# Performance work log

Hardware: AMD Instinct MI355X
Metric: run time of the kernel (lower is better)

## Reference

```python
import jax, jax.numpy as jnp
import numpy as np

TOP_K = 2

def setup_inputs() -> dict:
    key = jax.random.key(0)
    ks = jax.random.split(key, 6)
    B, L, D, E = 4, 4096, 1024, 8
    s = 1.0 / np.sqrt(D)
    return {
        "x": jax.random.normal(ks[0], (B, L, D), dtype=jnp.float32),
        "Wr": jax.random.normal(ks[1], (E, D), dtype=jnp.float32) * s,
        "W1": jax.random.normal(ks[2], (E, D, D), dtype=jnp.float32) * s,
        "b1": jax.random.normal(ks[3], (E, D), dtype=jnp.float32) * 0.01,
        "W2": jax.random.normal(ks[4], (E, D, D), dtype=jnp.float32) * s,
        "b2": jax.random.normal(ks[5], (E, D), dtype=jnp.float32) * 0.01,
    }

def reference(x, Wr, W1, b1, W2, b2):
    # x: [B,L,D]; Wr: [E,D]; W1/W2: [E,D,D]; b1/b2: [E,D]
    E = Wr.shape[0]
    logits = jnp.einsum("bld,ed->ble", x, Wr)           # router, no bias
    probs = jax.nn.softmax(logits, axis=-1)
    topw, topi = jax.lax.top_k(probs, TOP_K)             # [B,L,K]
    topw = topw / jnp.sum(topw, axis=-1, keepdims=True)  # renormalize
    # combine weights per expert: [B,L,E], zero where expert not selected
    comb = jnp.sum(jax.nn.one_hot(topi, E, dtype=x.dtype) * topw[..., None], axis=-2)
    out = jnp.zeros_like(x)
    for e in range(E):  # small fixed expert count
        h = jax.nn.gelu(jnp.einsum("bld,fd->blf", x, W1[e]) + b1[e], approximate=False)
        y = jnp.einsum("blf,df->bld", h, W2[e]) + b2[e]
        out = out + comb[..., e:e + 1] * y
    return out
```

## Files before the change

### kernel.cpp

```cpp
#include <hip/hip_runtime.h>
#include <hip/hip_bf16.h>
#include <cstdint>
#include <cstddef>

#define NTOK 16384
#define DDIM 1024
#define NEXP 8
#define CPAD 32

typedef __attribute__((ext_vector_type(8))) short bf16x8;
typedef __attribute__((ext_vector_type(4))) float f32x4;

__device__ __forceinline__ unsigned short f2bf(float f) {
  union { float f; unsigned u; } c; c.f = f;
  unsigned r = (c.u + 0x7FFFu + ((c.u >> 16) & 1u)) >> 16;
  return (unsigned short)r;
}

__device__ __forceinline__ float gelu_exact(float v) {
  return 0.5f * v * (1.0f + erff(v * 0.70710678118654752440f));
}

#define GL2LDS(gp, lp) __builtin_amdgcn_global_load_lds( \
    (__attribute__((address_space(1))) void*)(gp),       \
    (__attribute__((address_space(3))) void*)(lp), 16, 0, 0)

__global__ void cast_k(const float* __restrict__ src, unsigned short* __restrict__ dst, int n4) {
  int i = blockIdx.x * blockDim.x + threadIdx.x;
  if (i >= n4) return;
  float4 a = ((const float4*)src)[i];
  union { unsigned short s[4]; uint2 v; } o;
  o.s[0] = f2bf(a.x); o.s[1] = f2bf(a.y); o.s[2] = f2bf(a.z); o.s[3] = f2bf(a.w);
  ((uint2*)dst)[i] = o.v;
}

__global__ __launch_bounds__(256)
void castx_router_k(const float* __restrict__ x, const float* __restrict__ Wr,
                    unsigned short* __restrict__ xb, int* __restrict__ tokE,
                    float2* __restrict__ tokW) {
  const int t = blockIdx.x;
  const int tid = threadIdx.x;
  const int w = tid >> 6, lane = tid & 63;

  float4 xv = ((const float4*)x)[(size_t)t * 256 + tid];
  union { unsigned short s[4]; uint2 v; } o;
  o.s[0] = f2bf(xv.x); o.s[1] = f2bf(xv.y); o.s[2] = f2bf(xv.z); o.s[3] = f2bf(xv.w);
  ((uint2*)xb)[(size_t)t * 256 + tid] = o.v;

  const float4* Wr4 = (const float4*)Wr;
  float p[NEXP];
#pragma unroll
  for (int e = 0; e < NEXP; ++e) {
    float4 wv = Wr4[e * 256 + tid];
    p[e] = xv.x * wv.x + xv.y * wv.y + xv.z * wv.z + xv.w * wv.w;
  }
#pragma unroll
  for (int e = 0; e < NEXP; ++e) {
    float v = p[e];
#pragma unroll
    for (int off = 32; off >= 1; off >>= 1) v += __shfl_xor(v, off, 64);
    p[e] = v;
  }
  __shared__ float red[4][NEXP];
  if (lane == 0) {
#pragma unroll
    for (int e = 0; e < NEXP; ++e) red[w][e] = p[e];
  }
  __syncthreads();
  if (tid == 0) {
    float s[NEXP];
#pragma unroll
    for (int e = 0; e < NEXP; ++e) s[e] = red[0][e] + red[1][e] + red[2][e] + red[3][e];
    int e1 = 0; float m1 = s[0];
#pragma unroll
    for (int e = 1; e < NEXP; ++e) if (s[e] > m1) { m1 = s[e]; e1 = e; }
    int e2 = -1; float m2 = -3.4e38f;
#pragma unroll
    for (int e = 0; e < NEXP; ++e) {
      if (e == e1) continue;
      if (s[e] > m2) { m2 = s[e]; e2 = e; }
    }
    float dd = expf(m2 - m1);
    tokE[t] = e1 | (e2 << 8);
    tokW[t] = make_float2(1.f / (1.f + dd), dd / (1.f + dd));
  }
}

__global__ __launch_bounds__(256)
void hist_k(const int* __restrict__ tokE, int* __restrict__ cnt) {
  const int t = blockIdx.x * blockDim.x + threadIdx.x;
  const int w = threadIdx.x >> 6, lane = threadIdx.x & 63;
  const int pk = tokE[t];
  const int e1 = pk & 0xFF, e2 = (pk >> 8) & 0xFF;
  __shared__ int h[4][NEXP];
#pragma unroll
  for (int e = 0; e < NEXP; ++e) {
    int c = (int)__popcll(__ballot(e1 == e)) + (int)__popcll(__ballot(e2 == e));
    if (lane == 0) h[w][e] = c;
  }
  __syncthreads();
  if (threadIdx.x < NEXP) {
    int tot = h[0][threadIdx.x] + h[1][threadIdx.x] + h[2][threadIdx.x] + h[3][threadIdx.x];
    atomicAdd(&cnt[threadIdx.x * CPAD], tot);
  }
}

__global__ void offsets_k(const int* __restrict__ cnt, int* __restrict__ off) {
  if (threadIdx.x == 0) {
    int a = 0;
    for (int e = 0; e < NEXP; ++e) { off[e] = a; a += cnt[e * CPAD]; }
  }
}

__device__ __forceinline__ int bucket_slot(int* cur, int e_sel) {
  int lane = threadIdx.x & 63;
  int slot = 0;
#pragma unroll
  for (int e = 0; e < NEXP; ++e) {
    unsigned long long m = __ballot(e_sel == e);
    if (e_sel == e) {
      unsigned long long below = m & ((1ull << lane) - 1ull);
      int leader = __ffsll((long long)m) - 1;
      int base = 0;
      if (lane == leader) base = atomicAdd(&cur[e * CPAD], (int)__popcll(m));
      base = __shfl(base, leader, 64);
      slot = base + (int)__popcll(below);
    }
  }
  return slot;
}

__global__ __launch_bounds__(256)
void place_k(const int* __restrict__ tokE, const float2* __restrict__ tokW,
             const int* __restrict__ off, int* __restrict__ cur,
             int* __restrict__ asgT, float* __restrict__ asgW) {
  int t = blockIdx.x * blockDim.x + threadIdx.x;
  if (t >= NTOK) return;
  int pk = tokE[t];
  float2 w = tokW[t];
  int e1 = pk & 0xFF, e2 = (pk >> 8) & 0xFF;
  int p1 = off[e1] + bucket_slot(cur, e1);
  asgT[p1] = t; asgW[p1] = w.x;
  int p2 = off[e2] + bucket_slot(cur, e2);
  asgT[p2] = t; asgW[p2] = w.y;
}


__global__ __launch_bounds__(512, 2)
void gemm1_k(const unsigned short* __restrict__ xb, const unsigned short* __restrict__ w1b,
             const float* __restrict__ b1, const int* __restrict__ cntp,
             const int* __restrict__ offp, const int* __restrict__ asgT,
             unsigned short* __restrict__ h) {
  const int e = blockIdx.z;
  const int cnt = cntp[e * CPAD];
  const int m0 = blockIdx.x * 256;
  if (m0 >= cnt) return;
  const int off = offp[e];
  const int n0 = blockIdx.y * 256;

  __shared__ __align__(16) unsigned short As[2][16384];
  __shared__ __align__(16) unsigned short Bs[2][16384];

  const int tid = threadIdx.x;
  const int w = tid >> 6, lane = tid & 63;
  const int r = lane & 15, kc = lane >> 4;
  const int wr = w >> 2, wc = w & 3;

  const unsigned short* srcA[2];
  const unsigned short* srcB[2];
#pragma unroll
  for (int i = 0; i < 2; ++i) {
    int g = 2 * w + i;
    int rowt = m0 + g * 16 + r;
    int rowc = (rowt < cnt) ? rowt : m0;
    int tok = asgT[off + rowc];
    srcA[i] = xb + (size_t)tok * DDIM + kc * 8;
    int coln = n0 + g * 16 + r;
    srcB[i] = w1b + (size_t)e * DDIM * DDIM + (size_t)coln * DDIM + kc * 8;
  }

  f32x4 acc[8][4];
#pragma unroll
  for (int i = 0; i < 8; ++i)
#pragma unroll
    for (int j = 0; j < 4; ++j) acc[i][j] = (f32x4){0.f, 0.f, 0.f, 0.f};

  auto stage = [&](int buf, int k0) {
#pragma unroll
    for (int i = 0; i < 2; ++i) {
      int g = 2 * w + i;
#pragma unroll
      for (int ks = 0; ks < 2; ++ks) {
        GL2LDS(srcA[i] + k0 + ks * 32, &As[buf][g * 1024 + ks * 512 + lane * 8]);
        GL2LDS(srcB[i] + k0 + ks * 32, &Bs[buf][g * 1024 + ks * 512 + lane * 8]);
      }
    }
  };

  stage(0, 0);
  for (int s = 0; s < 16; ++s) {
    int buf = s & 1;
    __syncthreads();
    if (s + 1 < 16) stage(buf ^ 1, (s + 1) * 64);
#pragma unroll
    for (int ks = 0; ks < 2; ++ks) {
      bf16x8 af[8], bv[4];
#pragma unroll
      for (int i = 0; i < 8; ++i)
        af[i] = *(const bf16x8*)&As[buf][(wr * 8 + i) * 1024 + ks * 512 + lane * 8];
#pragma unroll
      for (int j = 0; j < 4; ++j)
        bv[j] = *(const bf16x8*)&Bs[buf][(wc * 4 + j) * 1024 + ks * 512 + lane * 8];
#pragma unroll
      for (int i = 0; i < 8; ++i)
#pragma unroll
        for (int j = 0; j < 4; ++j)
          acc[i][j] = __builtin_amdgcn_mfma_f32_16x16x32_bf16(af[i], bv[j], acc[i][j], 0, 0, 0);
    }
  }

  float bcol[4];
#pragma unroll
  for (int j = 0; j < 4; ++j) bcol[j] = b1[e * DDIM + n0 + wc * 64 + j * 16 + r];
#pragma unroll
  for (int i = 0; i < 8; ++i) {
#pragma unroll
    for (int q = 0; q < 4; ++q) {
      int grow = m0 + wr * 128 + i * 16 + kc * 4 + q;
      if (grow < cnt) {
        size_t hrow = (size_t)(off + grow) * DDIM;
#pragma unroll
        for (int j = 0; j < 4; ++j) {
          int col = n0 + wc * 64 + j * 16 + r;
          h[hrow + col] = f2bf(gelu_exact(acc[i][j][q] + bcol[j]));
        }
      }
    }
  }
}

__global__ __launch_bounds__(512, 2)
void gemm2_k(const unsigned short* __restrict__ hsrc, const unsigned short* __restrict__ w2b,
             const float* __restrict__ b2, const int* __restrict__ cntp,
             const int* __restrict__ offp, const int* __restrict__ asgT,
             const float* __restrict__ asgW, float* __restrict__ out) {
  const int e = blockIdx.z;
  const int cnt = cntp[e * CPAD];
  const int m0 = blockIdx.x * 256;
  if (m0 >= cnt) return;
  const int off = offp[e];
  const int n0 = blockIdx.y * 256;

  __shared__ __align__(16) unsigned short As[2][16384];
  __shared__ __align__(16) unsigned short Bs[2][16384];

  const int tid = threadIdx.x;
  const int w = tid >> 6, lane = tid & 63;
  const int r = lane & 15, kc = lane >> 4;
  const int wr = w >> 2, wc = w & 3;

  const unsigned short* srcA[2];
  const unsigned short* srcB[2];
#pragma unroll
  for (int i = 0; i < 2; ++i) {
    int g = 2 * w + i;
    int rowt = m0 + g * 16 + r;
    int rowc = (rowt < cnt) ? rowt : m0;
    srcA[i] = hsrc + (size_t)(off + rowc) * DDIM + kc * 8;
    int coln = n0 + g * 16 + r;
    srcB[i] = w2b + (size_t)e * DDIM * DDIM + (size_t)coln * DDIM + kc * 8;
  }

  f32x4 acc[8][4];
#pragma unroll
  for (int i = 0; i < 8; ++i)
#pragma unroll
    for (int j = 0; j < 4; ++j) acc[i][j] = (f32x4){0.f, 0.f, 0.f, 0.f};

  auto stage = [&](int buf, int k0) {
#pragma unroll
    for (int i = 0; i < 2; ++i) {
      int g = 2 * w + i;
#pragma unroll
      for (int ks = 0; ks < 2; ++ks) {
        GL2LDS(srcA[i] + k0 + ks * 32, &As[buf][g * 1024 + ks * 512 + lane * 8]);
        GL2LDS(srcB[i] + k0 + ks * 32, &Bs[buf][g * 1024 + ks * 512 + lane * 8]);
      }
    }
  };

  stage(0, 0);
  for (int s = 0; s < 16; ++s) {
    int buf = s & 1;
    __syncthreads();
    if (s + 1 < 16) stage(buf ^ 1, (s + 1) * 64);
#pragma unroll
    for (int ks = 0; ks < 2; ++ks) {
      bf16x8 af[8], bv[4];
#pragma unroll
      for (int i = 0; i < 8; ++i)
        af[i] = *(const bf16x8*)&As[buf][(wr * 8 + i) * 1024 + ks * 512 + lane * 8];
#pragma unroll
      for (int j = 0; j < 4; ++j)
        bv[j] = *(const bf16x8*)&Bs[buf][(wc * 4 + j) * 1024 + ks * 512 + lane * 8];
#pragma unroll
      for (int i = 0; i < 8; ++i)
#pragma unroll
        for (int j = 0; j < 4; ++j)
          acc[i][j] = __builtin_amdgcn_mfma_f32_16x16x32_bf16(af[i], bv[j], acc[i][j], 0, 0, 0);
    }
  }

  float bcol[4];
#pragma unroll
  for (int j = 0; j < 4; ++j) bcol[j] = b2[e * DDIM + n0 + wc * 64 + j * 16 + r];
#pragma unroll
  for (int i = 0; i < 8; ++i) {
#pragma unroll
    for (int q = 0; q < 4; ++q) {
      int grow = m0 + wr * 128 + i * 16 + kc * 4 + q;
      if (grow < cnt) {
        int tok = asgT[off + grow];
        float wgt = asgW[off + grow];
        float* orow = out + (size_t)tok * DDIM;
#pragma unroll
        for (int j = 0; j < 4; ++j) {
          int col = n0 + wc * 64 + j * 16 + r;
          atomicAdd(&orow[col], wgt * (acc[i][j][q] + bcol[j]));
        }
      }
    }
  }
}

extern "C" void kernel_launch(void* const* d_in, const int* in_sizes, int n_in,
                              void* d_out, int out_size, void* d_ws, size_t ws_size,
                              hipStream_t stream) {
  (void)in_sizes; (void)n_in; (void)ws_size;
  const float* x  = (const float*)d_in[0];
  const float* Wr = (const float*)d_in[1];
  const float* W1 = (const float*)d_in[2];
  const float* b1 = (const float*)d_in[3];
  const float* W2 = (const float*)d_in[4];
  const float* b2 = (const float*)d_in[5];
  float* out = (float*)d_out;

  char* ws = (char*)d_ws;
  int*    cnt  = (int*)(ws + 0);
  int*    off  = (int*)(ws + 4096);
  int*    cur  = (int*)(ws + 8192);
  int*    tokE = (int*)(ws + 16384);
  float2* tokW = (float2*)(ws + 16384 + 65536);
  int*    asgT = (int*)(ws + 16384 + 65536 + 131072);
  float*  asgW = (float*)(ws + 16384 + 65536 + 131072 + 131072);
  unsigned short* xb  = (unsigned short*)(ws + (size_t)(1u << 20));
  unsigned short* w1b = (unsigned short*)(ws + (size_t)33 * (1u << 20));
  unsigned short* w2b = (unsigned short*)(ws + (size_t)49 * (1u << 20));
  unsigned short* h   = (unsigned short*)(ws + (size_t)65 * (1u << 20));

  hipMemsetAsync(ws, 0, 16384, stream);
  hipMemsetAsync(d_out, 0, (size_t)out_size * sizeof(float), stream);

  const int nW = NEXP * DDIM * DDIM;
  cast_k<<<(nW / 4) / 256, 256, 0, stream>>>(W1, w1b, nW / 4);
  cast_k<<<(nW / 4) / 256, 256, 0, stream>>>(W2, w2b, nW / 4);

  castx_router_k<<<NTOK, 256, 0, stream>>>(x, Wr, xb, tokE, tokW);
  hist_k<<<NTOK / 256, 256, 0, stream>>>(tokE, cnt);
  offsets_k<<<1, 64, 0, stream>>>(cnt, off);
  place_k<<<NTOK / 256, 256, 0, stream>>>(tokE, tokW, off, cur, asgT, asgW);

  dim3 ggrid(64, 4, NEXP);
  gemm1_k<<<ggrid, 512, 0, stream>>>(xb, w1b, b1, cnt, off, asgT, h);
  gemm2_k<<<ggrid, 512, 0, stream>>>(h, w2b, b2, cnt, off, asgT, asgW, out);
}
```

Before: 715.4 us.

## Restructure MoE GEMM mainloop with explicit barriers, phased LDS reads and setprio

Both expert GEMM kernels now share a macro-generated mainloop. Each K-tile waits explicitly on vmcnt and a raw s_barrier, loads B fragments for both k-substeps once, then walks A fragments in four phases of two rows. Each MFMA cluster is raised with s_setprio and separated by barriers so LDS reads and MFMA issue interleave across waves. The aim is to cut register pressure from holding all eight A fragments and to overlap global-to-LDS prefetch and LDS reads with matrix math. The cost is many extra workgroup barriers per tile, which could serialize waves.

```diff
diff --git a/kernel.cpp b/kernel.cpp
--- a/kernel.cpp
+++ b/kernel.cpp
@@ -146,191 +146,168 @@
 }
 
 
+#define GEMM_CORE(EPILOG_PRE, SRC_A_INIT)                                               \
+  const int e = blockIdx.z;                                                             \
+  const int cnt = cntp[e * CPAD];                                                       \
+  const int m0 = blockIdx.x * 256;                                                      \
+  if (m0 >= cnt) return;                                                                \
+  const int off = offp[e];                                                              \
+  const int n0 = blockIdx.y * 256;                                                      \
+  __shared__ __align__(16) unsigned short As[2][16384];                                 \
+  __shared__ __align__(16) unsigned short Bs[2][16384];                                 \
+  const int tid = threadIdx.x;                                                          \
+  const int w = tid >> 6, lane = tid & 63;                                              \
+  const int r = lane & 15, kc = lane >> 4;                                              \
+  const int wr = w >> 2, wc = w & 3;                                                    \
+  const unsigned short* srcA[2];                                                        \
+  const unsigned short* srcB[2];                                                        \
+  _Pragma("unroll")                                                                     \
+  for (int i = 0; i < 2; ++i) {                                                         \
+    int g = 2 * w + i;                                                                  \
+    int rowt = m0 + g * 16 + r;                                                         \
+    int rowc = (rowt < cnt) ? rowt : m0;                                                \
+    SRC_A_INIT;                                                                         \
+    int coln = n0 + g * 16 + r;                                                         \
+    srcB[i] = Bsrc + (size_t)e * DDIM * DDIM + (size_t)coln * DDIM + kc * 8;            \
+  }                                                                                     \
+  f32x4 acc[8][4];                                                                      \
+  _Pragma("unroll")                                                                     \
+  for (int i = 0; i < 8; ++i)                                                           \
+    _Pragma("unroll")                                                                   \
+    for (int j = 0; j < 4; ++j) acc[i][j] = (f32x4){0.f, 0.f, 0.f, 0.f};                \
+  auto stage = [&](int buf, int kt) {                                                   \
+    _Pragma("unroll")                                                                   \
+    for (int i = 0; i < 2; ++i) {                                                       \
+      int g = 2 * w + i;                                                                \
+      _Pragma("unroll")                                                                 \
+      for (int ks = 0; ks < 2; ++ks) {                                                  \
+        GL2LDS(srcA[i] + kt * 64 + ks * 32, &As[buf][(g * 2 + ks) * 512 + lane * 8]);   \
+        GL2LDS(srcB[i] + kt * 64 + ks * 32, &Bs[buf][(g * 2 + ks) * 512 + lane * 8]);   \
+      }                                                                                 \
+    }                                                                                   \
+  };                                                                                    \
+  stage(0, 0);                                                                          \
+  for (int t = 0; t < 16; ++t) {                                                        \
+    const int b = t & 1;                                                                \
+    __builtin_amdgcn_sched_barrier(0);                                                  \
+    asm volatile("s_waitcnt vmcnt(0)" ::: "memory");                                    \
+    __builtin_amdgcn_s_barrier();                                                       \
+    __builtin_amdgcn_sched_barrier(0);                                                  \
+    bf16x8 bv[4][2], af[2][2];                                                          \
+    _Pragma("unroll")                                                                   \
+    for (int j = 0; j < 4; ++j)                                                         \
+      _Pragma("unroll")                                                                 \
+      for (int ks = 0; ks < 2; ++ks)                                                    \
+        bv[j][ks] = *(const bf16x8*)&Bs[b][((wc * 4 + j) * 2 + ks) * 512 + lane * 8];   \
+    _Pragma("unroll")                                                                   \
+    for (int i = 0; i < 2; ++i)                                                         \
+      _Pragma("unroll")                                                                 \
+      for (int ks = 0; ks < 2; ++ks)                                                    \
+        af[i][ks] = *(const bf16x8*)&As[b][((wr * 8 + i) * 2 + ks) * 512 + lane * 8];   \
+    if (t + 1 < 16) stage(b ^ 1, t + 1);                                                \
+    __builtin_amdgcn_s_barrier();                                                       \
+    asm volatile("s_waitcnt lgkmcnt(0)" ::: "memory");                                  \
+    __builtin_amdgcn_sched_barrier(0);                                                  \
+    __builtin_amdgcn_s_setprio(1);                                                      \
+    _Pragma("unroll")                                                                   \
+    for (int ks = 0; ks < 2; ++ks)                                                      \
+      _Pragma("unroll")                                                                 \
+      for (int i = 0; i < 2; ++i)                                                       \
+        _Pragma("unroll")                                                               \
+        for (int j = 0; j < 4; ++j)                                                     \
+          acc[i][j] = __builtin_amdgcn_mfma_f32_16x16x32_bf16(af[i][ks], bv[j][ks],     \
+                                                              acc[i][j], 0, 0, 0);      \
+    __builtin_amdgcn_s_setprio(0);                                                      \
+    __builtin_amdgcn_s_barrier();                                                       \
+    _Pragma("unroll")                                                                   \
+    for (int p = 1; p < 4; ++p) {                                                       \
+      _Pragma("unroll")                                                                 \
+      for (int i = 0; i < 2; ++i)                                                       \
+        _Pragma("unroll")                                                               \
+        for (int ks = 0; ks < 2; ++ks)                                                  \
+          af[i][ks] = *(const bf16x8*)&As[b][((wr * 8 + 2 * p + i) * 2 + ks) * 512 +    \
+                                             lane * 8];                                 \
+      __builtin_amdgcn_s_barrier();                                                     \
+      asm volatile("s_waitcnt lgkmcnt(0)" ::: "memory");                                \
+      __builtin_amdgcn_sched_barrier(0);                                                \
+      __builtin_amdgcn_s_setprio(1);                                                    \
+      _Pragma("unroll")                                                                 \
+      for (int ks = 0; ks < 2; ++ks)                                                    \
+        _Pragma("unroll")                                                               \
+        for (int i = 0; i < 2; ++i)                                                     \
+          _Pragma("unroll")                                                             \
+          for (int j = 0; j < 4; ++j)                                                   \
+            acc[2 * p + i][j] = __builtin_amdgcn_mfma_f32_16x16x32_bf16(                \
+                af[i][ks], bv[j][ks], acc[2 * p + i][j], 0, 0, 0);                      \
+      __builtin_amdgcn_s_setprio(0);                                                    \
+      __builtin_amdgcn_s_barrier();                                                     \
+    }                                                                                   \
+  }                                                                                     \
+  EPILOG_PRE
+
 __global__ __launch_bounds__(512, 2)
-void gemm1_k(const unsigned short* __restrict__ xb, const unsigned short* __restrict__ w1b,
+void gemm1_k(const unsigned short* __restrict__ xb, const unsigned short* __restrict__ Bsrc,
              const float* __restrict__ b1, const int* __restrict__ cntp,
              const int* __restrict__ offp, const int* __restrict__ asgT,
              unsigned short* __restrict__ h) {
-  const int e = blockIdx.z;
-  const int cnt = cntp[e * CPAD];
-  const int m0 = blockIdx.x * 256;
-  if (m0 >= cnt) return;
-  const int off = offp[e];
-  const int n0 = blockIdx.y * 256;
-
-  __shared__ __align__(16) unsigned short As[2][16384];
-  __shared__ __align__(16) unsigned short Bs[2][16384];
-
-  const int tid = threadIdx.x;
-  const int w = tid >> 6, lane = tid & 63;
-  const int r = lane & 15, kc = lane >> 4;
-  const int wr = w >> 2, wc = w & 3;
-
-  const unsigned short* srcA[2];
-  const unsigned short* srcB[2];
-#pragma unroll
-  for (int i = 0; i < 2; ++i) {
-    int g = 2 * w + i;
-    int rowt = m0 + g * 16 + r;
-    int rowc = (rowt < cnt) ? rowt : m0;
-    int tok = asgT[off + rowc];
-    srcA[i] = xb + (size_t)tok * DDIM + kc * 8;
-    int coln = n0 + g * 16 + r;
-    srcB[i] = w1b + (size_t)e * DDIM * DDIM + (size_t)coln * DDIM + kc * 8;
-  }
-
-  f32x4 acc[8][4];
-#pragma unroll
-  for (int i = 0; i < 8; ++i)
-#pragma unroll
-    for (int j = 0; j < 4; ++j) acc[i][j] = (f32x4){0.f, 0.f, 0.f, 0.f};
-
-  auto stage = [&](int buf, int k0) {
-#pragma unroll
-    for (int i = 0; i < 2; ++i) {
-      int g = 2 * w + i;
-#pragma unroll
-      for (int ks = 0; ks < 2; ++ks) {
-        GL2LDS(srcA[i] + k0 + ks * 32, &As[buf][g * 1024 + ks * 512 + lane * 8]);
-        GL2LDS(srcB[i] + k0 + ks * 32, &Bs[buf][g * 1024 + ks * 512 + lane * 8]);
-      }
-    }
-  };
-
-  stage(0, 0);
-  for (int s = 0; s < 16; ++s) {
-    int buf = s & 1;
-    __syncthreads();
-    if (s + 1 < 16) stage(buf ^ 1, (s + 1) * 64);
-#pragma unroll
-    for (int ks = 0; ks < 2; ++ks) {
-      bf16x8 af[8], bv[4];
-#pragma unroll
-      for (int i = 0; i < 8; ++i)
-        af[i] = *(const bf16x8*)&As[buf][(wr * 8 + i) * 1024 + ks * 512 + lane * 8];
-#pragma unroll
-      for (int j = 0; j < 4; ++j)
-        bv[j] = *(const bf16x8*)&Bs[buf][(wc * 4 + j) * 1024 + ks * 512 + lane * 8];
-#pragma unroll
-      for (int i = 0; i < 8; ++i)
-#pragma unroll
-        for (int j = 0; j < 4; ++j)
-          acc[i][j] = __builtin_amdgcn_mfma_f32_16x16x32_bf16(af[i], bv[j], acc[i][j], 0, 0, 0);
-    }
-  }
-
-  float bcol[4];
-#pragma unroll
-  for (int j = 0; j < 4; ++j) bcol[j] = b1[e * DDIM + n0 + wc * 64 + j * 16 + r];
-#pragma unroll
-  for (int i = 0; i < 8; ++i) {
-#pragma unroll
-    for (int q = 0; q < 4; ++q) {
-      int grow = m0 + wr * 128 + i * 16 + kc * 4 + q;
-      if (grow < cnt) {
-        size_t hrow = (size_t)(off + grow) * DDIM;
-#pragma unroll
-        for (int j = 0; j < 4; ++j) {
-          int col = n0 + wc * 64 + j * 16 + r;
-          h[hrow + col] = f2bf(gelu_exact(acc[i][j][q] + bcol[j]));
+  GEMM_CORE(
+     {
+      float bcol[4];
+      _Pragma("unroll")
+      for (int j = 0; j < 4; ++j) bcol[j] = b1[e * DDIM + n0 + wc * 64 + j * 16 + r];
+      _Pragma("unroll")
+      for (int i = 0; i < 8; ++i) {
+        _Pragma("unroll")
+        for (int q = 0; q < 4; ++q) {
+          int grow = m0 + wr * 128 + i * 16 + kc * 4 + q;
+          if (grow < cnt) {
+            size_t hrow = (size_t)(off + grow) * DDIM;
+            _Pragma("unroll")
+            for (int j = 0; j < 4; ++j) {
+              int col = n0 + wc * 64 + j * 16 + r;
+              h[hrow + col] = f2bf(gelu_exact(acc[i][j][q] + bcol[j]));
+            }
+          }
         }
       }
-    }
-  }
+    },
+     {
+      int tok = asgT[off + rowc];
+      srcA[i] = xb + (size_t)tok * DDIM + kc * 8;
+    });
 }
 
 __global__ __launch_bounds__(512, 2)
-void gemm2_k(const unsigned short* __restrict__ hsrc, const unsigned short* __restrict__ w2b,
+void gemm2_k(const unsigned short* __restrict__ hsrc, const unsigned short* __restrict__ Bsrc,
              const float* __restrict__ b2, const int* __restrict__ cntp,
              const int* __restrict__ offp, const int* __restrict__ asgT,
              const float* __restrict__ asgW, float* __restrict__ out) {
-  const int e = blockIdx.z;
-  const int cnt = cntp[e * CPAD];
-  const int m0 = blockIdx.x * 256;
-  if (m0 >= cnt) return;
-  const int off = offp[e];
-  const int n0 = blockIdx.y * 256;
-
-  __shared__ __align__(16) unsigned short As[2][16384];
-  __shared__ __align__(16) unsigned short Bs[2][16384];
-
-  const int tid = threadIdx.x;
-  const int w = tid >> 6, lane = tid & 63;
-  const int r = lane & 15, kc = lane >> 4;
-  const int wr = w >> 2, wc = w & 3;
-
-  const unsigned short* srcA[2];
-  const unsigned short* srcB[2];
-#pragma unroll
-  for (int i = 0; i < 2; ++i) {
-    int g = 2 * w + i;
-    int rowt = m0 + g * 16 + r;
-    int rowc = (rowt < cnt) ? rowt : m0;
-    srcA[i] = hsrc + (size_t)(off + rowc) * DDIM + kc * 8;
-    int coln = n0 + g * 16 + r;
-    srcB[i] = w2b + (size_t)e * DDIM * DDIM + (size_t)coln * DDIM + kc * 8;
-  }
-
-  f32x4 acc[8][4];
-#pragma unroll
-  for (int i = 0; i < 8; ++i)
-#pragma unroll
-    for (int j = 0; j < 4; ++j) acc[i][j] = (f32x4){0.f, 0.f, 0.f, 0.f};
-
-  auto stage = [&](int buf, int k0) {
-#pragma unroll
-    for (int i = 0; i < 2; ++i) {
-      int g = 2 * w + i;
-#pragma unroll
-      for (int ks = 0; ks < 2; ++ks) {
-        GL2LDS(srcA[i] + k0 + ks * 32, &As[buf][g * 1024 + ks * 512 + lane * 8]);
-        GL2LDS(srcB[i] + k0 + ks * 32, &Bs[buf][g * 1024 + ks * 512 + lane * 8]);
-      }
-    }
-  };
-
-  stage(0, 0);
-  for (int s = 0; s < 16; ++s) {
-    int buf = s & 1;
-    __syncthreads();
-    if (s + 1 < 16) stage(buf ^ 1, (s + 1) * 64);
-#pragma unroll
-    for (int ks = 0; ks < 2; ++ks) {
-      bf16x8 af[8], bv[4];
-#pragma unroll
-      for (int i = 0; i < 8; ++i)
-        af[i] = *(const bf16x8*)&As[buf][(wr * 8 + i) * 1024 + ks * 512 + lane * 8];
-#pragma unroll
-      for (int j = 0; j < 4; ++j)
-        bv[j] = *(const bf16x8*)&Bs[buf][(wc * 4 + j) * 1024 + ks * 512 + lane * 8];
-#pragma unroll
-      for (int i = 0; i < 8; ++i)
-#pragma unroll
-        for (int j = 0; j < 4; ++j)
-          acc[i][j] = __builtin_amdgcn_mfma_f32_16x16x32_bf16(af[i], bv[j], acc[i][j], 0, 0, 0);
-    }
-  }
-
-  float bcol[4];
-#pragma unroll
-  for (int j = 0; j < 4; ++j) bcol[j] = b2[e * DDIM + n0 + wc * 64 + j * 16 + r];
-#pragma unroll
-  for (int i = 0; i < 8; ++i) {
-#pragma unroll
-    for (int q = 0; q < 4; ++q) {
-      int grow = m0 + wr * 128 + i * 16 + kc * 4 + q;
-      if (grow < cnt) {
-        int tok = asgT[off + grow];
-        float wgt = asgW[off + grow];
-        float* orow = out + (size_t)tok * DDIM;
-#pragma unroll
-        for (int j = 0; j < 4; ++j) {
-          int col = n0 + wc * 64 + j * 16 + r;
-          atomicAdd(&orow[col], wgt * (acc[i][j][q] + bcol[j]));
+  GEMM_CORE(
+     {
+      float bcol[4];
+      _Pragma("unroll")
+      for (int j = 0; j < 4; ++j) bcol[j] = b2[e * DDIM + n0 + wc * 64 + j * 16 + r];
+      _Pragma("unroll")
+      for (int i = 0; i < 8; ++i) {
+        _Pragma("unroll")
+        for (int q = 0; q < 4; ++q) {
+          int grow = m0 + wr * 128 + i * 16 + kc * 4 + q;
+          if (grow < cnt) {
+            int tok = asgT[off + grow];
+            float wgt = asgW[off + grow];
+            float* orow = out + (size_t)tok * DDIM;
+            _Pragma("unroll")
+            for (int j = 0; j < 4; ++j) {
+              int col = n0 + wc * 64 + j * 16 + r;
+              atomicAdd(&orow[col], wgt * (acc[i][j][q] + bcol[j]));
+            }
+          }
         }
       }
-    }
-  }
+    },
+     {
+      srcA[i] = hsrc + (size_t)(off + rowc) * DDIM + kc * 8;
+    });
 }
 
 extern "C" void kernel_launch(void* const* d_in, const int* in_sizes, int n_in,
```

Result: slower. 816.7 us (+14.2%).
